# Performance work log

Measured on AMD Instinct MI355X. Metric: run time of the kernel, lower is better.

The kernel has to match this reference:

```python
import jax, jax.numpy as jnp
import numpy as np

N, IN_DIM, HID, NCLS = 100000, 512, 128, 10
ALPHA = 0.2  # LeakyReLU negative slope

def _xavier_normal(key, shape, gain=1.414):
    fan_in, fan_out = shape[0], shape[1]
    std = gain * (2.0 / (fan_in + fan_out)) ** 0.5
    return (jax.random.normal(key, shape, jnp.float32) * std).astype(jnp.float32)

def setup_inputs() -> dict:
    key = jax.random.key(0)
    k1, k2, k3, k4, k5, k6 = jax.random.split(key, 6)
    features = jax.random.normal(k1, (N, IN_DIM), jnp.float32)
    # learned params per init_kwargs (xavier_normal with gain=1.414 as in torch)
    C = _xavier_normal(k2, (IN_DIM, HID))
    W = _xavier_normal(k3, (2 * HID, HID))
    V = _xavier_normal(k4, (HID, NCLS))
    # per-node top-2 neighbors from sortNodes(weight_dict[idx]); the buggy
    # `while len(...) < 2` loop never runs, so only the first merge matters.
    n1_idx = jax.random.randint(k5, (N,), 0, N, dtype=jnp.int64 if jax.config.read('jax_enable_x64') else jnp.int32)
    n2_idx = jax.random.randint(k6, (N,), 0, N, dtype=n1_idx.dtype)
    return {"features": features, "C": C, "W": W, "V": V,
            "n1_idx": n1_idx, "n2_idx": n2_idx}

def reference(features, C, W, V, n1_idx, n2_idx):
    # h = features @ C : [N, H]
    h = features @ C
    # For every node, the effective output of the Huffman merge loop is the
    # single merge of its two top-sorted neighbors (duplicated if degree 1):
    # concat(h[n1], h[n2]) @ W. Split W into halves to avoid materializing [N, 2H].
    W1, W2 = W[:HID], W[HID:]                      # each [H, H]
    outs = h[n1_idx] @ W1 + h[n2_idx] @ W2         # [N, H]
    results = jax.nn.leaky_relu(outs @ V, negative_slope=ALPHA)  # [N, num_class]
    return jax.nn.log_softmax(results, axis=1)
```

## Files before the change

### kernel.cpp

```cpp
#include <hip/hip_runtime.h>
#include <hip/hip_bf16.h>
#include <stdint.h>

#define NROWS 100000
#define INDIM 512
#define HID 128
#define NCLS 10
#define LEAKY_ALPHA 0.2f
#define GSTR 24

typedef __bf16 bf16x8_t __attribute__((ext_vector_type(8)));
typedef __bf16 bf16x4_t __attribute__((ext_vector_type(4)));
typedef float f32x4_t __attribute__((ext_vector_type(4)));
typedef unsigned short ushort8_t __attribute__((ext_vector_type(8)));

union Frag {
    bf16x8_t v8;
    bf16x4_t v4[2];
    unsigned short u[8];
};

__device__ __forceinline__ unsigned short f2bf(float x) {
    union { __hip_bfloat16 b; unsigned short u; } cv;
    cv.b = __float2bfloat16(x);
    return cv.u;
}

__device__ __forceinline__ int img_addr(int r, int kk) {
    int p = r >> 1;
    int o = ((r & 1) << 6) | (kk << 1);
    return (p << 7) | ((((o >> 4) ^ (p & 7)) << 4) | (o & 15));
}

__device__ __forceinline__ void gload_lds16(const void* g, void* l) {
    __builtin_amdgcn_global_load_lds(
        (const __attribute__((address_space(1))) unsigned int*)g,
        (__attribute__((address_space(3))) unsigned int*)l, 16, 0, 0);
}

__global__ __launch_bounds__(256) void k_prep(
    const float* __restrict__ C, const float* __restrict__ W, const float* __restrict__ V,
    unsigned short* __restrict__ Qimg) {
    __shared__ float Vl[HID * NCLS];
    __shared__ float Pl[2][HID][10];
    __shared__ float Cl[32][132];

    const int tid = threadIdx.x, b = blockIdx.x;
    for (int i = tid; i < HID * NCLS; i += 256) Vl[i] = V[i];
    __syncthreads();

    {
        const int half = tid >> 7, j = tid & 127;
        const float* wr = W + (half * HID + j) * HID;
        float s[NCLS];
#pragma unroll
        for (int c = 0; c < NCLS; ++c) s[c] = 0.f;
        for (int m = 0; m < HID; m += 4) {
            float4 wv = *reinterpret_cast<const float4*>(wr + m);
            float wa[4] = {wv.x, wv.y, wv.z, wv.w};
#pragma unroll
            for (int u = 0; u < 4; ++u)
#pragma unroll
                for (int c = 0; c < NCLS; ++c) s[c] += wa[u] * Vl[(m + u) * NCLS + c];
        }
#pragma unroll
        for (int c = 0; c < NCLS; ++c) Pl[half][j][c] = s[c];
    }
    const int k0 = b << 5;
    {
        const int kr = tid >> 3, ns = (tid & 7) << 4;
        const float4* src = reinterpret_cast<const float4*>(C + (k0 + kr) * HID + ns);
#pragma unroll
        for (int j = 0; j < 4; ++j)
            *reinterpret_cast<float4*>(&Cl[kr][ns + 4 * j]) = src[j];
    }
    __syncthreads();

    for (int e = tid; e < 32 * 32; e += 256) {
        const int n = e >> 5, kl = e & 31;
        const int half = n >> 4, c = n & 15;
        float s = 0.f;
        if (c < NCLS) {
#pragma unroll 4
            for (int j = 0; j < HID; ++j) s += Cl[kl][j] * Pl[half][j][c];
        }
        *(unsigned short*)((char*)Qimg + b * 2048 + img_addr(n, kl)) = f2bf(s);
    }
}

__global__ __launch_bounds__(256, 3) void k_gemm(
    const float* __restrict__ A,
    const unsigned short* __restrict__ Qimg,
    float* __restrict__ G)
{
    __shared__ unsigned short Qs[16384];
    __shared__ unsigned short As[2][4096];

    const int tid  = threadIdx.x;
    const int w    = tid >> 6;
    const int lane = tid & 63;
    const int l15  = lane & 15;
    const int kg   = (lane >> 4) << 2;
    const long row0 = (long)blockIdx.x * 128;

#pragma unroll
    for (int j = 0; j < 8; ++j) {
        const int off = (j * 4 + w) * 1024;
        gload_lds16((const char*)Qimg + off + lane * 16, (char*)Qs + off);
    }

    const int ar_s = tid >> 1;
    const int kh   = (tid & 1) << 4;
    long gr = row0 + ar_s;
    if (gr >= NROWS) gr = NROWS - 1;
    const float* asrc = A + gr * INDIM + kh;
    const int aw0 = img_addr(ar_s, kh);
    const int aw1 = img_addr(ar_s, kh + 8);

    int ard0[2], ard1[2], brd0[2], brd1[2];
#pragma unroll
    for (int ii = 0; ii < 2; ++ii) {
        int r = w * 32 + ii * 16 + l15;
        ard0[ii] = img_addr(r, kg);
        ard1[ii] = img_addr(r, kg + 16);
    }
#pragma unroll
    for (int f = 0; f < 2; ++f) {
        brd0[f] = img_addr(f * 16 + l15, kg);
        brd1[f] = img_addr(f * 16 + l15, kg + 16);
    }

    f32x4_t acc[2][2];
#pragma unroll
    for (int i = 0; i < 2; ++i)
#pragma unroll
        for (int f = 0; f < 2; ++f)
#pragma unroll
            for (int r = 0; r < 4; ++r) acc[i][f][r] = 0.f;

    const char* asb = (const char*)&As[0][0];
    const char* bsb = (const char*)&Qs[0];

    float4 qA[4], qB[4], qC[4];

    {
        float4 v[4];
#pragma unroll
        for (int j = 0; j < 4; ++j) v[j] = *reinterpret_cast<const float4*>(asrc + 4 * j);
        ushort8_t lo, hi;
#pragma unroll
        for (int e = 0; e < 4; ++e) {
            lo[e] = f2bf(v[0][e]); lo[4 + e] = f2bf(v[1][e]);
            hi[e] = f2bf(v[2][e]); hi[4 + e] = f2bf(v[3][e]);
        }
        *(ushort8_t*)((char*)asb + aw0) = lo;
        *(ushort8_t*)((char*)asb + aw1) = hi;
    }
#pragma unroll
    for (int j = 0; j < 4; ++j) qB[j] = *reinterpret_cast<const float4*>(asrc + 32 + 4 * j);
#pragma unroll
    for (int j = 0; j < 4; ++j) qC[j] = *reinterpret_cast<const float4*>(asrc + 64 + 4 * j);
#pragma unroll
    for (int j = 0; j < 4; ++j) qA[j] = *reinterpret_cast<const float4*>(asrc + 96 + 4 * j);
    __syncthreads();

#pragma unroll
    for (int t = 0; t < 16; ++t) {
        const int cur = t & 1;

        Frag fa[2], fb[2];
#pragma unroll
        for (int ii = 0; ii < 2; ++ii) {
            fa[ii].v4[0] = *(const bf16x4_t*)(asb + cur * 8192 + ard0[ii]);
            fa[ii].v4[1] = *(const bf16x4_t*)(asb + cur * 8192 + ard1[ii]);
        }
#pragma unroll
        for (int f = 0; f < 2; ++f) {
            fb[f].v4[0] = *(const bf16x4_t*)(bsb + t * 2048 + brd0[f]);
            fb[f].v4[1] = *(const bf16x4_t*)(bsb + t * 2048 + brd1[f]);
        }
#pragma unroll
        for (int ii = 0; ii < 2; ++ii)
#pragma unroll
            for (int f = 0; f < 2; ++f)
                acc[ii][f] = __builtin_amdgcn_mfma_f32_16x16x32_bf16(fa[ii].v8, fb[f].v8, acc[ii][f], 0, 0, 0);

        if (t < 15) {
            const int slot = (t + 1) % 3;
            ushort8_t lo, hi;
            if (slot == 0) {
#pragma unroll
                for (int e = 0; e < 4; ++e) {
                    lo[e] = f2bf(qA[0][e]); lo[4 + e] = f2bf(qA[1][e]);
                    hi[e] = f2bf(qA[2][e]); hi[4 + e] = f2bf(qA[3][e]);
                }
            } else if (slot == 1) {
#pragma unroll
                for (int e = 0; e < 4; ++e) {
                    lo[e] = f2bf(qB[0][e]); lo[4 + e] = f2bf(qB[1][e]);
                    hi[e] = f2bf(qB[2][e]); hi[4 + e] = f2bf(qB[3][e]);
                }
            } else {
#pragma unroll
                for (int e = 0; e < 4; ++e) {
                    lo[e] = f2bf(qC[0][e]); lo[4 + e] = f2bf(qC[1][e]);
                    hi[e] = f2bf(qC[2][e]); hi[4 + e] = f2bf(qC[3][e]);
                }
            }
            *(ushort8_t*)((char*)asb + (cur ^ 1) * 8192 + aw0) = lo;
            *(ushort8_t*)((char*)asb + (cur ^ 1) * 8192 + aw1) = hi;

            if (t + 4 <= 15) {
                const float* src = asrc + (t + 4) * 32;
                if (slot == 0) {
#pragma unroll
                    for (int j = 0; j < 4; ++j) qA[j] = *reinterpret_cast<const float4*>(src + 4 * j);
                } else if (slot == 1) {
#pragma unroll
                    for (int j = 0; j < 4; ++j) qB[j] = *reinterpret_cast<const float4*>(src + 4 * j);
                } else {
#pragma unroll
                    for (int j = 0; j < 4; ++j) qC[j] = *reinterpret_cast<const float4*>(src + 4 * j);
                }
            }
        }
    }

    const int rq_ = (lane >> 4) << 2;
#pragma unroll
    for (int ii = 0; ii < 2; ++ii)
#pragma unroll
        for (int r = 0; r < 4; ++r) {
            long grow = row0 + w * 32 + ii * 16 + rq_ + r;
            if (l15 < NCLS && grow < NROWS) {
                G[grow * GSTR + l15]      = acc[ii][0][r];
                G[grow * GSTR + 12 + l15] = acc[ii][1][r];
            }
        }
}

__global__ __launch_bounds__(256) void k_epi(
    const float* __restrict__ G,
    const int* __restrict__ n1, const int* __restrict__ n2,
    float* __restrict__ Out) {
    const long i = (long)blockIdx.x * 256 + threadIdx.x;
    if (i >= NROWS) return;
    const float* g1 = G + (long)n1[i] * GSTR;
    const float* g2 = G + (long)n2[i] * GSTR + 12;

    float4 a0 = *(const float4*)(g1);
    float4 a1 = *(const float4*)(g1 + 4);
    float2 a2 = *(const float2*)(g1 + 8);
    float4 b0 = *(const float4*)(g2);
    float4 b1 = *(const float4*)(g2 + 4);
    float2 b2 = *(const float2*)(g2 + 8);

    float x[NCLS] = {a0.x + b0.x, a0.y + b0.y, a0.z + b0.z, a0.w + b0.w,
                     a1.x + b1.x, a1.y + b1.y, a1.z + b1.z, a1.w + b1.w,
                     a2.x + b2.x, a2.y + b2.y};
    float m = -1e30f;
#pragma unroll
    for (int c = 0; c < NCLS; ++c) {
        x[c] = (x[c] >= 0.f) ? x[c] : LEAKY_ALPHA * x[c];
        m = fmaxf(m, x[c]);
    }
    float sum = 0.f;
#pragma unroll
    for (int c = 0; c < NCLS; ++c) sum += __expf(x[c] - m);
    const float lse = m + __logf(sum);
    float2* o = (float2*)(Out + i * NCLS);
#pragma unroll
    for (int j = 0; j < 5; ++j) {
        float2 v = {x[2 * j] - lse, x[2 * j + 1] - lse};
        o[j] = v;
    }
}

extern "C" void kernel_launch(void* const* d_in, const int* in_sizes, int n_in,
                              void* d_out, int out_size, void* d_ws, size_t ws_size,
                              hipStream_t stream) {
    const float* features = (const float*)d_in[0];
    const float* C  = (const float*)d_in[1];
    const float* W  = (const float*)d_in[2];
    const float* V  = (const float*)d_in[3];
    const int*   n1 = (const int*)d_in[4];
    const int*   n2 = (const int*)d_in[5];
    float* out = (float*)d_out;

    char* ws = (char*)d_ws;
    unsigned short* Qimg = (unsigned short*)ws;
    float* G = (float*)(ws + 32768);

    hipLaunchKernelGGL(k_prep, dim3(16), dim3(256), 0, stream, C, W, V, Qimg);
    hipLaunchKernelGGL(k_gemm, dim3((NROWS + 127) / 128), dim3(256), 0, stream,
                       features, Qimg, G);
    hipLaunchKernelGGL(k_epi, dim3((NROWS + 255) / 256), dim3(256), 0, stream,
                       G, n1, n2, out);
}
```

Baseline: 64.07 us.

## Store intermediate G in bf16, single-buffer A tile, stagger K order per block

The intermediate G (per-row projected logits for both neighbor halves) is now stored as bf16 with a 32-element stride instead of fp32 with stride 24, halving the bytes written by the GEMM and gathered by the epilogue. The GEMM A tile in LDS drops from double to single buffering, the register prefetch goes from three slots to two, and the occupancy hint rises from 3 to 4 blocks per CU. Each block also starts its K loop at a different offset (blockIdx mod 16) to spread DRAM and channel access. The single LDS buffer is written right after being read within an iteration with no barrier, which risks a read/write race, and bf16 storage of G loses precision.

```diff
diff --git a/kernel.cpp b/kernel.cpp
--- a/kernel.cpp
+++ b/kernel.cpp
@@ -7,7 +7,6 @@
 #define HID 128
 #define NCLS 10
 #define LEAKY_ALPHA 0.2f
-#define GSTR 24
 
 typedef __bf16 bf16x8_t __attribute__((ext_vector_type(8)));
 typedef __bf16 bf16x4_t __attribute__((ext_vector_type(4)));
@@ -24,6 +23,12 @@
     union { __hip_bfloat16 b; unsigned short u; } cv;
     cv.b = __float2bfloat16(x);
     return cv.u;
+}
+
+__device__ __forceinline__ float bf2f(unsigned short u) {
+    union { float f; unsigned int i; } v;
+    v.i = ((unsigned int)u) << 16;
+    return v.f;
 }
 
 __device__ __forceinline__ int img_addr(int r, int kk) {
@@ -88,13 +93,13 @@
     }
 }
 
-__global__ __launch_bounds__(256, 3) void k_gemm(
+__global__ __launch_bounds__(256, 4) void k_gemm(
     const float* __restrict__ A,
     const unsigned short* __restrict__ Qimg,
-    float* __restrict__ G)
+    unsigned short* __restrict__ G)
 {
     __shared__ unsigned short Qs[16384];
-    __shared__ unsigned short As[2][4096];
+    __shared__ unsigned short As[4096];
 
     const int tid  = threadIdx.x;
     const int w    = tid >> 6;
@@ -102,6 +107,7 @@
     const int l15  = lane & 15;
     const int kg   = (lane >> 4) << 2;
     const long row0 = (long)blockIdx.x * 128;
+    const int phase = blockIdx.x & 15;
 
 #pragma unroll
     for (int j = 0; j < 8; ++j) {
@@ -138,15 +144,16 @@
 #pragma unroll
             for (int r = 0; r < 4; ++r) acc[i][f][r] = 0.f;
 
-    const char* asb = (const char*)&As[0][0];
+    const char* asb = (const char*)&As[0];
     const char* bsb = (const char*)&Qs[0];
 
-    float4 qA[4], qB[4], qC[4];
-
-    {
+    float4 qA[4], qB[4];
+
+    {
+        const float* s0 = asrc + ((0 + phase) & 15) * 32;
         float4 v[4];
 #pragma unroll
-        for (int j = 0; j < 4; ++j) v[j] = *reinterpret_cast<const float4*>(asrc + 4 * j);
+        for (int j = 0; j < 4; ++j) v[j] = *reinterpret_cast<const float4*>(s0 + 4 * j);
         ushort8_t lo, hi;
 #pragma unroll
         for (int e = 0; e < 4; ++e) {
@@ -156,28 +163,30 @@
         *(ushort8_t*)((char*)asb + aw0) = lo;
         *(ushort8_t*)((char*)asb + aw1) = hi;
     }
-#pragma unroll
-    for (int j = 0; j < 4; ++j) qB[j] = *reinterpret_cast<const float4*>(asrc + 32 + 4 * j);
-#pragma unroll
-    for (int j = 0; j < 4; ++j) qC[j] = *reinterpret_cast<const float4*>(asrc + 64 + 4 * j);
-#pragma unroll
-    for (int j = 0; j < 4; ++j) qA[j] = *reinterpret_cast<const float4*>(asrc + 96 + 4 * j);
+    {
+        const float* s1 = asrc + ((1 + phase) & 15) * 32;
+#pragma unroll
+        for (int j = 0; j < 4; ++j) qB[j] = *reinterpret_cast<const float4*>(s1 + 4 * j);
+        const float* s2 = asrc + ((2 + phase) & 15) * 32;
+#pragma unroll
+        for (int j = 0; j < 4; ++j) qA[j] = *reinterpret_cast<const float4*>(s2 + 4 * j);
+    }
     __syncthreads();
 
 #pragma unroll
     for (int t = 0; t < 16; ++t) {
-        const int cur = t & 1;
+        const int pt = (t + phase) & 15;
 
         Frag fa[2], fb[2];
 #pragma unroll
         for (int ii = 0; ii < 2; ++ii) {
-            fa[ii].v4[0] = *(const bf16x4_t*)(asb + cur * 8192 + ard0[ii]);
-            fa[ii].v4[1] = *(const bf16x4_t*)(asb + cur * 8192 + ard1[ii]);
+            fa[ii].v4[0] = *(const bf16x4_t*)(asb + ard0[ii]);
+            fa[ii].v4[1] = *(const bf16x4_t*)(asb + ard1[ii]);
         }
 #pragma unroll
         for (int f = 0; f < 2; ++f) {
-            fb[f].v4[0] = *(const bf16x4_t*)(bsb + t * 2048 + brd0[f]);
-            fb[f].v4[1] = *(const bf16x4_t*)(bsb + t * 2048 + brd1[f]);
+            fb[f].v4[0] = *(const bf16x4_t*)(bsb + pt * 2048 + brd0[f]);
+            fb[f].v4[1] = *(const bf16x4_t*)(bsb + pt * 2048 + brd1[f]);
         }
 #pragma unroll
         for (int ii = 0; ii < 2; ++ii)
@@ -186,15 +195,9 @@
                 acc[ii][f] = __builtin_amdgcn_mfma_f32_16x16x32_bf16(fa[ii].v8, fb[f].v8, acc[ii][f], 0, 0, 0);
 
         if (t < 15) {
-            const int slot = (t + 1) % 3;
+            const int slot = (t + 1) & 1;
             ushort8_t lo, hi;
-            if (slot == 0) {
-#pragma unroll
-                for (int e = 0; e < 4; ++e) {
-                    lo[e] = f2bf(qA[0][e]); lo[4 + e] = f2bf(qA[1][e]);
-                    hi[e] = f2bf(qA[2][e]); hi[4 + e] = f2bf(qA[3][e]);
-                }
-            } else if (slot == 1) {
+            if (slot == 1) {
 #pragma unroll
                 for (int e = 0; e < 4; ++e) {
                     lo[e] = f2bf(qB[0][e]); lo[4 + e] = f2bf(qB[1][e]);
@@ -203,24 +206,21 @@
             } else {
 #pragma unroll
                 for (int e = 0; e < 4; ++e) {
-                    lo[e] = f2bf(qC[0][e]); lo[4 + e] = f2bf(qC[1][e]);
-                    hi[e] = f2bf(qC[2][e]); hi[4 + e] = f2bf(qC[3][e]);
+                    lo[e] = f2bf(qA[0][e]); lo[4 + e] = f2bf(qA[1][e]);
+                    hi[e] = f2bf(qA[2][e]); hi[4 + e] = f2bf(qA[3][e]);
                 }
             }
-            *(ushort8_t*)((char*)asb + (cur ^ 1) * 8192 + aw0) = lo;
-            *(ushort8_t*)((char*)asb + (cur ^ 1) * 8192 + aw1) = hi;
-
-            if (t + 4 <= 15) {
-                const float* src = asrc + (t + 4) * 32;
-                if (slot == 0) {
-#pragma unroll
-                    for (int j = 0; j < 4; ++j) qA[j] = *reinterpret_cast<const float4*>(src + 4 * j);
-                } else if (slot == 1) {
+            *(ushort8_t*)((char*)asb + aw0) = lo;
+            *(ushort8_t*)((char*)asb + aw1) = hi;
+
+            if (t + 3 <= 15) {
+                const float* src = asrc + (((t + 3) + phase) & 15) * 32;
+                if (slot == 1) {
 #pragma unroll
                     for (int j = 0; j < 4; ++j) qB[j] = *reinterpret_cast<const float4*>(src + 4 * j);
                 } else {
 #pragma unroll
-                    for (int j = 0; j < 4; ++j) qC[j] = *reinterpret_cast<const float4*>(src + 4 * j);
+                    for (int j = 0; j < 4; ++j) qA[j] = *reinterpret_cast<const float4*>(src + 4 * j);
                 }
             }
         }
@@ -233,31 +233,29 @@
         for (int r = 0; r < 4; ++r) {
             long grow = row0 + w * 32 + ii * 16 + rq_ + r;
             if (l15 < NCLS && grow < NROWS) {
-                G[grow * GSTR + l15]      = acc[ii][0][r];
-                G[grow * GSTR + 12 + l15] = acc[ii][1][r];
+                G[grow * 32 + l15]      = f2bf(acc[ii][0][r]);
+                G[grow * 32 + 16 + l15] = f2bf(acc[ii][1][r]);
             }
         }
 }
 
 __global__ __launch_bounds__(256) void k_epi(
-    const float* __restrict__ G,
+    const unsigned short* __restrict__ G,
     const int* __restrict__ n1, const int* __restrict__ n2,
     float* __restrict__ Out) {
     const long i = (long)blockIdx.x * 256 + threadIdx.x;
     if (i >= NROWS) return;
-    const float* g1 = G + (long)n1[i] * GSTR;
-    const float* g2 = G + (long)n2[i] * GSTR + 12;
-
-    float4 a0 = *(const float4*)(g1);
-    float4 a1 = *(const float4*)(g1 + 4);
-    float2 a2 = *(const float2*)(g1 + 8);
-    float4 b0 = *(const float4*)(g2);
-    float4 b1 = *(const float4*)(g2 + 4);
-    float2 b2 = *(const float2*)(g2 + 8);
-
-    float x[NCLS] = {a0.x + b0.x, a0.y + b0.y, a0.z + b0.z, a0.w + b0.w,
-                     a1.x + b1.x, a1.y + b1.y, a1.z + b1.z, a1.w + b1.w,
-                     a2.x + b2.x, a2.y + b2.y};
+    const ushort8_t* p1 = (const ushort8_t*)(G + (long)n1[i] * 32);
+    const ushort8_t* p2 = (const ushort8_t*)(G + (long)n2[i] * 32 + 16);
+    ushort8_t a0 = p1[0], a1 = p1[1];
+    ushort8_t b0 = p2[0], b1 = p2[1];
+
+    float x[NCLS];
+#pragma unroll
+    for (int c = 0; c < 8; ++c) x[c] = bf2f(a0[c]) + bf2f(b0[c]);
+    x[8] = bf2f(a1[0]) + bf2f(b1[0]);
+    x[9] = bf2f(a1[1]) + bf2f(b1[1]);
+
     float m = -1e30f;
 #pragma unroll
     for (int c = 0; c < NCLS; ++c) {
@@ -289,7 +287,7 @@
 
     char* ws = (char*)d_ws;
     unsigned short* Qimg = (unsigned short*)ws;
-    float* G = (float*)(ws + 32768);
+    unsigned short* G = (unsigned short*)(ws + 32768);
 
     hipLaunchKernelGGL(k_prep, dim3(16), dim3(256), 0, stream, C, W, V, Qimg);
     hipLaunchKernelGGL(k_gemm, dim3((NROWS + 127) / 128), dim3(256), 0, stream,
```

Result: slower. 67.08 us (+4.7%).

## Stage A in K=128 chunks with wide register prefetch instead of K=32 ring

Applied to the files above, without the earlier changes.

The GEMM kernel now loads 128 K-columns of each A row per round, 16 float4 per thread, converts them to bf16 and writes four K=32 LDS slices at once, for four rounds in total. This replaces the sixteen-step loop that used a three-slot register ring and a double-buffered LDS tile. The aim is to put more global bytes in flight per load round and to cut per-step control overhead. In exchange the A tile in LDS grows to 32KB and launch bounds drop from 3 to 2 blocks per CU, which lowers occupancy and leaves less room to hide memory latency.

```diff
diff --git a/kernel.cpp b/kernel.cpp
--- a/kernel.cpp
+++ b/kernel.cpp
@@ -88,13 +88,13 @@
     }
 }
 
-__global__ __launch_bounds__(256, 3) void k_gemm(
+__global__ __launch_bounds__(256, 2) void k_gemm(
     const float* __restrict__ A,
     const unsigned short* __restrict__ Qimg,
     float* __restrict__ G)
 {
     __shared__ unsigned short Qs[16384];
-    __shared__ unsigned short As[2][4096];
+    __shared__ unsigned short As[16384];
 
     const int tid  = threadIdx.x;
     const int w    = tid >> 6;
@@ -110,12 +110,15 @@
     }
 
     const int ar_s = tid >> 1;
-    const int kh   = (tid & 1) << 4;
+    const int hk   = (tid & 1) << 6;
     long gr = row0 + ar_s;
     if (gr >= NROWS) gr = NROWS - 1;
-    const float* asrc = A + gr * INDIM + kh;
-    const int aw0 = img_addr(ar_s, kh);
-    const int aw1 = img_addr(ar_s, kh + 8);
+    const float* asrc = A + gr * INDIM + hk;
+    const int s0 = hk >> 5;
+    int awr[8];
+#pragma unroll
+    for (int u = 0; u < 8; ++u)
+        awr[u] = (s0 + (u >> 2)) * 8192 + img_addr(ar_s, (u & 3) * 8);
 
     int ard0[2], ard1[2], brd0[2], brd1[2];
 #pragma unroll
@@ -138,90 +141,66 @@
 #pragma unroll
             for (int r = 0; r < 4; ++r) acc[i][f][r] = 0.f;
 
-    const char* asb = (const char*)&As[0][0];
+    const char* asb = (const char*)&As[0];
     const char* bsb = (const char*)&Qs[0];
 
-    float4 qA[4], qB[4], qC[4];
-
     {
-        float4 v[4];
-#pragma unroll
-        for (int j = 0; j < 4; ++j) v[j] = *reinterpret_cast<const float4*>(asrc + 4 * j);
-        ushort8_t lo, hi;
-#pragma unroll
-        for (int e = 0; e < 4; ++e) {
-            lo[e] = f2bf(v[0][e]); lo[4 + e] = f2bf(v[1][e]);
-            hi[e] = f2bf(v[2][e]); hi[4 + e] = f2bf(v[3][e]);
-        }
-        *(ushort8_t*)((char*)asb + aw0) = lo;
-        *(ushort8_t*)((char*)asb + aw1) = hi;
-    }
-#pragma unroll
-    for (int j = 0; j < 4; ++j) qB[j] = *reinterpret_cast<const float4*>(asrc + 32 + 4 * j);
-#pragma unroll
-    for (int j = 0; j < 4; ++j) qC[j] = *reinterpret_cast<const float4*>(asrc + 64 + 4 * j);
-#pragma unroll
-    for (int j = 0; j < 4; ++j) qA[j] = *reinterpret_cast<const float4*>(asrc + 96 + 4 * j);
+        float4 v[16];
+#pragma unroll
+        for (int j = 0; j < 16; ++j) v[j] = *reinterpret_cast<const float4*>(asrc + 4 * j);
+#pragma unroll
+        for (int u = 0; u < 8; ++u) {
+            ushort8_t pk;
+#pragma unroll
+            for (int e = 0; e < 4; ++e) {
+                pk[e]     = f2bf(v[2 * u][e]);
+                pk[4 + e] = f2bf(v[2 * u + 1][e]);
+            }
+            *(ushort8_t*)((char*)asb + awr[u]) = pk;
+        }
+    }
     __syncthreads();
 
 #pragma unroll
-    for (int t = 0; t < 16; ++t) {
-        const int cur = t & 1;
-
-        Frag fa[2], fb[2];
-#pragma unroll
-        for (int ii = 0; ii < 2; ++ii) {
-            fa[ii].v4[0] = *(const bf16x4_t*)(asb + cur * 8192 + ard0[ii]);
-            fa[ii].v4[1] = *(const bf16x4_t*)(asb + cur * 8192 + ard1[ii]);
-        }
-#pragma unroll
-        for (int f = 0; f < 2; ++f) {
-            fb[f].v4[0] = *(const bf16x4_t*)(bsb + t * 2048 + brd0[f]);
-            fb[f].v4[1] = *(const bf16x4_t*)(bsb + t * 2048 + brd1[f]);
-        }
-#pragma unroll
-        for (int ii = 0; ii < 2; ++ii)
-#pragma unroll
-            for (int f = 0; f < 2; ++f)
-                acc[ii][f] = __builtin_amdgcn_mfma_f32_16x16x32_bf16(fa[ii].v8, fb[f].v8, acc[ii][f], 0, 0, 0);
-
-        if (t < 15) {
-            const int slot = (t + 1) % 3;
-            ushort8_t lo, hi;
-            if (slot == 0) {
+    for (int t = 0; t < 4; ++t) {
+        float4 nx[16];
+        if (t < 3) {
+            const float* src = asrc + (t + 1) * 128;
+#pragma unroll
+            for (int j = 0; j < 16; ++j) nx[j] = *reinterpret_cast<const float4*>(src + 4 * j);
+        }
+
+#pragma unroll
+        for (int s = 0; s < 4; ++s) {
+            Frag fa[2], fb[2];
+#pragma unroll
+            for (int ii = 0; ii < 2; ++ii) {
+                fa[ii].v4[0] = *(const bf16x4_t*)(asb + s * 8192 + ard0[ii]);
+                fa[ii].v4[1] = *(const bf16x4_t*)(asb + s * 8192 + ard1[ii]);
+            }
+            const int qt = t * 4 + s;
+#pragma unroll
+            for (int f = 0; f < 2; ++f) {
+                fb[f].v4[0] = *(const bf16x4_t*)(bsb + qt * 2048 + brd0[f]);
+                fb[f].v4[1] = *(const bf16x4_t*)(bsb + qt * 2048 + brd1[f]);
+            }
+#pragma unroll
+            for (int ii = 0; ii < 2; ++ii)
+#pragma unroll
+                for (int f = 0; f < 2; ++f)
+                    acc[ii][f] = __builtin_amdgcn_mfma_f32_16x16x32_bf16(fa[ii].v8, fb[f].v8, acc[ii][f], 0, 0, 0);
+        }
+
+        if (t < 3) {
+#pragma unroll
+            for (int u = 0; u < 8; ++u) {
+                ushort8_t pk;
 #pragma unroll
                 for (int e = 0; e < 4; ++e) {
-                    lo[e] = f2bf(qA[0][e]); lo[4 + e] = f2bf(qA[1][e]);
-                    hi[e] = f2bf(qA[2][e]); hi[4 + e] = f2bf(qA[3][e]);
+                    pk[e]     = f2bf(nx[2 * u][e]);
+                    pk[4 + e] = f2bf(nx[2 * u + 1][e]);
                 }
-            } else if (slot == 1) {
-#pragma unroll
-                for (int e = 0; e < 4; ++e) {
-                    lo[e] = f2bf(qB[0][e]); lo[4 + e] = f2bf(qB[1][e]);
-                    hi[e] = f2bf(qB[2][e]); hi[4 + e] = f2bf(qB[3][e]);
-                }
-            } else {
-#pragma unroll
-                for (int e = 0; e < 4; ++e) {
-                    lo[e] = f2bf(qC[0][e]); lo[4 + e] = f2bf(qC[1][e]);
-                    hi[e] = f2bf(qC[2][e]); hi[4 + e] = f2bf(qC[3][e]);
-                }
-            }
-            *(ushort8_t*)((char*)asb + (cur ^ 1) * 8192 + aw0) = lo;
-            *(ushort8_t*)((char*)asb + (cur ^ 1) * 8192 + aw1) = hi;
-
-            if (t + 4 <= 15) {
-                const float* src = asrc + (t + 4) * 32;
-                if (slot == 0) {
-#pragma unroll
-                    for (int j = 0; j < 4; ++j) qA[j] = *reinterpret_cast<const float4*>(src + 4 * j);
-                } else if (slot == 1) {
-#pragma unroll
-                    for (int j = 0; j < 4; ++j) qB[j] = *reinterpret_cast<const float4*>(src + 4 * j);
-                } else {
-#pragma unroll
-                    for (int j = 0; j < 4; ++j) qC[j] = *reinterpret_cast<const float4*>(src + 4 * j);
-                }
+                *(ushort8_t*)((char*)asb + awr[u]) = pk;
             }
         }
     }
```

Result: slower. 71.69 us (+11.9%).

## Fuse prep, GEMM and epilogue into one persistent cooperative kernel

Applied to the files above, without the earlier changes.

Merges the three launches into a single cooperative kernel with grid-wide syncs between the prep, GEMM and gather/log-softmax phases. The grid is sized from occupancy (assuming 256 CUs) and loops persistently over row tiles, staging the Q image into LDS only once per block. This removes two kernel launch gaps and the repeated Q staging. In exchange it adds grid.sync overhead and a host-side attribute and occupancy query on every call, and keeps the old three-kernel path as a fallback.

```diff
diff --git a/kernel.cpp b/kernel.cpp
--- a/kernel.cpp
+++ b/kernel.cpp
@@ -1,6 +1,9 @@
 #include <hip/hip_runtime.h>
+#include <hip/hip_cooperative_groups.h>
 #include <hip/hip_bf16.h>
 #include <stdint.h>
+
+namespace cg = cooperative_groups;
 
 #define NROWS 100000
 #define INDIM 512
@@ -8,6 +11,7 @@
 #define NCLS 10
 #define LEAKY_ALPHA 0.2f
 #define GSTR 24
+#define NTILES ((NROWS + 127) / 128)
 
 typedef __bf16 bf16x8_t __attribute__((ext_vector_type(8)));
 typedef __bf16 bf16x4_t __attribute__((ext_vector_type(4)));
@@ -38,17 +42,17 @@
         (__attribute__((address_space(3))) unsigned int*)l, 16, 0, 0);
 }
 
-__global__ __launch_bounds__(256) void k_prep(
+
+struct PrepSm { float Vl[HID * NCLS]; float Pl[2][HID][10]; float Cl[32][132]; };
+struct MainSm { unsigned short Qs[16384]; unsigned short As[2][4096]; };
+union SMem { PrepSm p; MainSm m; };
+
+__device__ __forceinline__ void prep_body(
+    PrepSm& sm, int b, int tid,
     const float* __restrict__ C, const float* __restrict__ W, const float* __restrict__ V,
     unsigned short* __restrict__ Qimg) {
-    __shared__ float Vl[HID * NCLS];
-    __shared__ float Pl[2][HID][10];
-    __shared__ float Cl[32][132];
-
-    const int tid = threadIdx.x, b = blockIdx.x;
-    for (int i = tid; i < HID * NCLS; i += 256) Vl[i] = V[i];
+    for (int i = tid; i < HID * NCLS; i += 256) sm.Vl[i] = V[i];
     __syncthreads();
-
     {
         const int half = tid >> 7, j = tid & 127;
         const float* wr = W + (half * HID + j) * HID;
@@ -61,10 +65,10 @@
 #pragma unroll
             for (int u = 0; u < 4; ++u)
 #pragma unroll
-                for (int c = 0; c < NCLS; ++c) s[c] += wa[u] * Vl[(m + u) * NCLS + c];
-        }
-#pragma unroll
-        for (int c = 0; c < NCLS; ++c) Pl[half][j][c] = s[c];
+                for (int c = 0; c < NCLS; ++c) s[c] += wa[u] * sm.Vl[(m + u) * NCLS + c];
+        }
+#pragma unroll
+        for (int c = 0; c < NCLS; ++c) sm.Pl[half][j][c] = s[c];
     }
     const int k0 = b << 5;
     {
@@ -72,41 +76,37 @@
         const float4* src = reinterpret_cast<const float4*>(C + (k0 + kr) * HID + ns);
 #pragma unroll
         for (int j = 0; j < 4; ++j)
-            *reinterpret_cast<float4*>(&Cl[kr][ns + 4 * j]) = src[j];
+            *reinterpret_cast<float4*>(&sm.Cl[kr][ns + 4 * j]) = src[j];
     }
     __syncthreads();
-
     for (int e = tid; e < 32 * 32; e += 256) {
         const int n = e >> 5, kl = e & 31;
         const int half = n >> 4, c = n & 15;
         float s = 0.f;
         if (c < NCLS) {
 #pragma unroll 4
-            for (int j = 0; j < HID; ++j) s += Cl[kl][j] * Pl[half][j][c];
+            for (int j = 0; j < HID; ++j) s += sm.Cl[kl][j] * sm.Pl[half][j][c];
         }
         *(unsigned short*)((char*)Qimg + b * 2048 + img_addr(n, kl)) = f2bf(s);
     }
 }
 
-__global__ __launch_bounds__(256, 3) void k_gemm(
-    const float* __restrict__ A,
-    const unsigned short* __restrict__ Qimg,
-    float* __restrict__ G)
-{
-    __shared__ unsigned short Qs[16384];
-    __shared__ unsigned short As[2][4096];
-
-    const int tid  = threadIdx.x;
+__device__ __forceinline__ void gemm_tile(
+    MainSm& sm, int tile, bool stage_q, int tid,
+    const float* __restrict__ A, const unsigned short* __restrict__ Qimg,
+    float* __restrict__ G) {
     const int w    = tid >> 6;
     const int lane = tid & 63;
     const int l15  = lane & 15;
     const int kg   = (lane >> 4) << 2;
-    const long row0 = (long)blockIdx.x * 128;
-
-#pragma unroll
-    for (int j = 0; j < 8; ++j) {
-        const int off = (j * 4 + w) * 1024;
-        gload_lds16((const char*)Qimg + off + lane * 16, (char*)Qs + off);
+    const long row0 = (long)tile * 128;
+
+    if (stage_q) {
+#pragma unroll
+        for (int j = 0; j < 8; ++j) {
+            const int off = (j * 4 + w) * 1024;
+            gload_lds16((const char*)Qimg + off + lane * 16, (char*)sm.Qs + off);
+        }
     }
 
     const int ar_s = tid >> 1;
@@ -138,8 +138,8 @@
 #pragma unroll
             for (int r = 0; r < 4; ++r) acc[i][f][r] = 0.f;
 
-    const char* asb = (const char*)&As[0][0];
-    const char* bsb = (const char*)&Qs[0];
+    const char* asb = (const char*)&sm.As[0][0];
+    const char* bsb = (const char*)&sm.Qs[0];
 
     float4 qA[4], qB[4], qC[4];
 
@@ -162,12 +162,12 @@
     for (int j = 0; j < 4; ++j) qC[j] = *reinterpret_cast<const float4*>(asrc + 64 + 4 * j);
 #pragma unroll
     for (int j = 0; j < 4; ++j) qA[j] = *reinterpret_cast<const float4*>(asrc + 96 + 4 * j);
-    __syncthreads();
+
+    if (stage_q) __syncthreads();
 
 #pragma unroll
     for (int t = 0; t < 16; ++t) {
         const int cur = t & 1;
-
         Frag fa[2], fb[2];
 #pragma unroll
         for (int ii = 0; ii < 2; ++ii) {
@@ -239,12 +239,10 @@
         }
 }
 
-__global__ __launch_bounds__(256) void k_epi(
-    const float* __restrict__ G,
+__device__ __forceinline__ void epi_row(
+    long i, const float* __restrict__ G,
     const int* __restrict__ n1, const int* __restrict__ n2,
     float* __restrict__ Out) {
-    const long i = (long)blockIdx.x * 256 + threadIdx.x;
-    if (i >= NROWS) return;
     const float* g1 = G + (long)n1[i] * GSTR;
     const float* g2 = G + (long)n2[i] * GSTR + 12;
 
@@ -274,6 +272,56 @@
         float2 v = {x[2 * j] - lse, x[2 * j + 1] - lse};
         o[j] = v;
     }
+}
+
+__global__ __launch_bounds__(256, 3) void k_fused(
+    const float* __restrict__ A, const float* __restrict__ C,
+    const float* __restrict__ W, const float* __restrict__ V,
+    const int* __restrict__ n1, const int* __restrict__ n2,
+    unsigned short* __restrict__ Qimg, float* __restrict__ G,
+    float* __restrict__ Out) {
+    __shared__ SMem sm;
+    const int tid = threadIdx.x;
+    cg::grid_group grid = cg::this_grid();
+
+    if (blockIdx.x < 16) {
+        prep_body(sm.p, blockIdx.x, tid, C, W, V, Qimg);
+        __threadfence();
+    }
+    grid.sync();
+
+    bool first = true;
+    for (int tile = blockIdx.x; tile < NTILES; tile += gridDim.x) {
+        gemm_tile(sm.m, tile, first, tid, A, Qimg, G);
+        first = false;
+    }
+    __threadfence();
+    grid.sync();
+
+    for (long i = (long)blockIdx.x * 256 + tid; i < NROWS; i += (long)gridDim.x * 256)
+        epi_row(i, G, n1, n2, Out);
+}
+
+__global__ __launch_bounds__(256) void k_prep(
+    const float* __restrict__ C, const float* __restrict__ W, const float* __restrict__ V,
+    unsigned short* __restrict__ Qimg) {
+    __shared__ PrepSm sm;
+    prep_body(sm, blockIdx.x, threadIdx.x, C, W, V, Qimg);
+}
+
+__global__ __launch_bounds__(256, 3) void k_gemm(
+    const float* __restrict__ A, const unsigned short* __restrict__ Qimg,
+    float* __restrict__ G) {
+    __shared__ MainSm sm;
+    gemm_tile(sm, blockIdx.x, true, threadIdx.x, A, Qimg, G);
+}
+
+__global__ __launch_bounds__(256) void k_epi(
+    const float* __restrict__ G,
+    const int* __restrict__ n1, const int* __restrict__ n2,
+    float* __restrict__ Out) {
+    const long i = (long)blockIdx.x * 256 + threadIdx.x;
+    if (i < NROWS) epi_row(i, G, n1, n2, Out);
 }
 
 extern "C" void kernel_launch(void* const* d_in, const int* in_sizes, int n_in,
@@ -291,9 +339,23 @@
     unsigned short* Qimg = (unsigned short*)ws;
     float* G = (float*)(ws + 32768);
 
+    int coop = 0, dev = 0;
+    hipGetDevice(&dev);
+    hipDeviceGetAttribute(&coop, hipDeviceAttributeCooperativeLaunch, dev);
+    int nb = 0;
+    if (coop &&
+        hipOccupancyMaxActiveBlocksPerMultiprocessor(&nb, k_fused, 256, 0) == hipSuccess &&
+        nb >= 1) {
+        int grid = nb * 256;
+        if (grid > NTILES) grid = NTILES;
+        void* args[9] = {(void*)&features, (void*)&C, (void*)&W, (void*)&V,
+                         (void*)&n1, (void*)&n2, (void*)&Qimg, (void*)&G, (void*)&out};
+        if (hipLaunchCooperativeKernel((const void*)k_fused, dim3(grid), dim3(256),
+                                       args, 0, stream) == hipSuccess)
+            return;
+    }
     hipLaunchKernelGGL(k_prep, dim3(16), dim3(256), 0, stream, C, W, V, Qimg);
-    hipLaunchKernelGGL(k_gemm, dim3((NROWS + 127) / 128), dim3(256), 0, stream,
-                       features, Qimg, G);
+    hipLaunchKernelGGL(k_gemm, dim3(NTILES), dim3(256), 0, stream, features, Qimg, G);
     hipLaunchKernelGGL(k_epi, dim3((NROWS + 255) / 256), dim3(256), 0, stream,
                        G, n1, n2, out);
 }
```

After: 158.2 us. 147% more time.
